# Performance work log

Hardware: AMD Instinct MI355X
Metric: run time of the kernel (lower is better)

Reference implementation:

```python
import jax, jax.numpy as jnp
import numpy as np

N_HEADS = 8
PROJ_DIM = 32


def _phi(x):
    # elu(x) + 1 feature map (always > 0)
    return jax.nn.elu(x) + 1.0


def _causal_linear(pq, pk, v):
    # Faithful to torch _linear_kernelized_attention masked branch:
    #   dpq_l = pq_l - pq_{l-1} (with pq_{-1}=0)
    #   result_l = cumsum_{m<=l} (dpq_m . v_m) * pk_m
    # The torch code materializes (N,H,L,D,D); here the identical math is
    # computed via a per-position scalar c_m = dpq_m . v_m, O(L*D) memory.
    dpq = pq - jnp.concatenate([jnp.zeros_like(pq[..., :1, :]), pq[..., :-1, :]], axis=-2)
    c = jnp.einsum('nhld,nhld->nhl', dpq, v)[..., None]  # (N,H,L,1)
    return jnp.cumsum(c * pk, axis=-2)  # (N,H,L,D)


def _bidir_linear(pq, pk, v):
    # Non-masked linear path: (pk^T v) first, then pq @ (.)
    right = jnp.einsum('nhld,nhle->nhde', pk, v)
    return jnp.einsum('nhqd,nhde->nhqe', pq, right)


def _attention(Y, X, Wq, Wk, Wv, mask):
    N, Lq, Dm = Y.shape
    Lk = X.shape[1]
    H, Pd = N_HEADS, PROJ_DIM
    # torch Linear: x @ W^T
    q = (Y @ Wq.T).reshape(N, Lq, H, Pd).transpose(0, 2, 1, 3)  # (N,H,Lq,Pd)
    k = (X @ Wk.T).reshape(N, Lk, H, Pd).transpose(0, 2, 1, 3)
    v = (X @ Wv.T).reshape(N, Lk, H, Pd).transpose(0, 2, 1, 3)
    pq, pk = _phi(q), _phi(k)
    fn = _causal_linear if mask else _bidir_linear
    num = fn(pq, pk, v)
    den = fn(pq, pk, jnp.ones_like(v))  # v_scale = ones expanded to D
    A = num / den
    return A.transpose(0, 2, 1, 3).reshape(N, Lq, H * Pd)


def setup_inputs() -> dict:
    key = jax.random.key(0)
    kY, kX, kq, kk, kv = jax.random.split(key, 5)
    N, L, dim = 2, 8192, N_HEADS * PROJ_DIM
    scale_in = 0.05            # keep phi(q),phi(k) ~ 1 so denominator stays positive
    scale_w = 1.0 / np.sqrt(dim)
    Y = scale_in * jax.random.normal(kY, (N, L, dim), dtype=jnp.float32)
    X = scale_in * jax.random.normal(kX, (N, L, dim), dtype=jnp.float32)
    Wq = scale_w * jax.random.normal(kq, (dim, dim), dtype=jnp.float32)
    Wk = scale_w * jax.random.normal(kk, (dim, dim), dtype=jnp.float32)
    Wv = scale_w * jax.random.normal(kv, (dim, dim), dtype=jnp.float32)
    return {"Y": Y, "X": X, "Wq": Wq, "Wk": Wk, "Wv": Wv, "mask": 1}


def reference(Y, X, Wq, Wk, Wv, mask):
    return _attention(Y, X, Wq, Wk, Wv, mask)
```

## Files before the change

### kernel.cpp

```cpp
#include <hip/hip_runtime.h>
#include <hip/hip_bf16.h>


typedef __attribute__((ext_vector_type(8))) short short8;
typedef __attribute__((ext_vector_type(4))) float f32x4;

__device__ __forceinline__ float phi_f(float x) {
    return x > 0.f ? x + 1.f : __expf(x);
}
__device__ __forceinline__ unsigned short f2bf(float x) {
    __hip_bfloat16 h = __float2bfloat16(x);
    return *reinterpret_cast<unsigned short*>(&h);
}
__device__ __forceinline__ float bf2f(unsigned short u) {
    return __uint_as_float(((unsigned int)u) << 16);
}

__global__ __launch_bounds__(256) void k_prepw(
        const float* __restrict__ Wq, const float* __restrict__ Wk,
        const float* __restrict__ Wv, unsigned short* __restrict__ Wf)
{
    const int g = blockIdx.x * 256 + threadIdx.x;
    const int mat = g >> 13, cc = g & 8191;
    const float* src = (mat == 0) ? Wq : (mat == 1 ? Wv : Wk);
    const int ln = cc & 15, qd = (cc >> 4) & 3, kt = (cc >> 6) & 7, jt = cc >> 9;
    const float* s = src + (size_t)(jt * 16 + ln) * 256 + kt * 32 + qd * 8;
    float4 f0 = *(const float4*)s, f1 = *(const float4*)(s + 4);
    short8 o;
    o[0] = f2bf(f0.x); o[1] = f2bf(f0.y); o[2] = f2bf(f0.z); o[3] = f2bf(f0.w);
    o[4] = f2bf(f1.x); o[5] = f2bf(f1.y); o[6] = f2bf(f1.z); o[7] = f2bf(f1.w);
    *(short8*)(Wf + (size_t)g * 8) = o;
}

#define LDA 280

__global__ __launch_bounds__(512, 4) void k_gemm(
        const float* __restrict__ Y, const float* __restrict__ X,
        const unsigned short* __restrict__ Wf,
        unsigned short* __restrict__ pk_out,
        float* __restrict__ c_out, float* __restrict__ cd_out,
        float* __restrict__ tot)
{
    __shared__ __align__(16) unsigned short Ys[33 * LDA];
    __shared__ __align__(16) unsigned short Xs[32 * LDA];
    __shared__ float scc[32][8], scd[32][8];
    __shared__ __align__(16) unsigned short spk[32 * 264];

    const int rb = blockIdx.x;
    const int n = rb >> 8, tile = rb & 255;
    const int mbase = rb * 32, lseg0 = tile * 32;
    const bool hasprev = (tile != 0);
    const int t = threadIdx.x, w = t >> 6, lane = t & 63;
    const int ln = lane & 15, qd = lane >> 4;

#pragma unroll
    for (int it = 0; it < 8; ++it) {
        const int idx = t + it * 512;
        const int half = idx >> 11, row = (idx >> 6) & 31, c4 = idx & 63;
        const float* s = (half ? X : Y) + (size_t)(mbase + row) * 256 + c4 * 4;
        float4 f = *(const float4*)s;
        ushort4 h4;
        h4.x = f2bf(f.x); h4.y = f2bf(f.y); h4.z = f2bf(f.z); h4.w = f2bf(f.w);
        unsigned short* dst = half ? Xs : Ys;
        *(ushort4*)&dst[row * LDA + c4 * 4] = h4;
    }
    if (t < 64) {
        const int prow = hasprev ? mbase - 1 : mbase;
        float4 f = *(const float4*)(Y + (size_t)prow * 256 + t * 4);
        ushort4 h4;
        h4.x = f2bf(f.x); h4.y = f2bf(f.y); h4.z = f2bf(f.z); h4.w = f2bf(f.w);
        *(ushort4*)&Ys[32 * LDA + t * 4] = h4;
    }
    __syncthreads();

    f32x4 aq[2][2], av[2][2], akk[2][2], aqp[2];
#pragma unroll
    for (int i = 0; i < 2; ++i)
#pragma unroll
        for (int j = 0; j < 2; ++j) {
            aq[i][j]  = (f32x4){0.f, 0.f, 0.f, 0.f};
            av[i][j]  = (f32x4){0.f, 0.f, 0.f, 0.f};
            akk[i][j] = (f32x4){0.f, 0.f, 0.f, 0.f};
        }
    aqp[0] = (f32x4){0.f, 0.f, 0.f, 0.f};
    aqp[1] = (f32x4){0.f, 0.f, 0.f, 0.f};
    const short8 z8 = {0, 0, 0, 0, 0, 0, 0, 0};
    const short8* W8 = (const short8*)Wf;

#pragma unroll
    for (int kt = 0; kt < 8; ++kt) {
        const int ko = kt * 32 + qd * 8;
        short8 ay0 = *(const short8*)&Ys[ln * LDA + ko];
        short8 ay1 = *(const short8*)&Ys[(16 + ln) * LDA + ko];
        short8 ax0 = *(const short8*)&Xs[ln * LDA + ko];
        short8 ax1 = *(const short8*)&Xs[(16 + ln) * LDA + ko];
        short8 ext = *(const short8*)&Ys[32 * LDA + ko];
        short8 ayp = (ln == 15) ? ext : z8;
#pragma unroll
        for (int jj = 0; jj < 2; ++jj) {
            const int jt = w * 2 + jj;
            short8 bq = W8[(((0 * 16 + jt) * 8 + kt) << 6) + lane];
            short8 bv = W8[(((1 * 16 + jt) * 8 + kt) << 6) + lane];
            short8 bk = W8[(((2 * 16 + jt) * 8 + kt) << 6) + lane];
            aq[0][jj]  = __builtin_amdgcn_mfma_f32_16x16x32_bf16(ay0, bq, aq[0][jj], 0, 0, 0);
            aq[1][jj]  = __builtin_amdgcn_mfma_f32_16x16x32_bf16(ay1, bq, aq[1][jj], 0, 0, 0);
            aqp[jj]    = __builtin_amdgcn_mfma_f32_16x16x32_bf16(ayp, bq, aqp[jj], 0, 0, 0);
            av[0][jj]  = __builtin_amdgcn_mfma_f32_16x16x32_bf16(ax0, bv, av[0][jj], 0, 0, 0);
            av[1][jj]  = __builtin_amdgcn_mfma_f32_16x16x32_bf16(ax1, bv, av[1][jj], 0, 0, 0);
            akk[0][jj] = __builtin_amdgcn_mfma_f32_16x16x32_bf16(ax0, bk, akk[0][jj], 0, 0, 0);
            akk[1][jj] = __builtin_amdgcn_mfma_f32_16x16x32_bf16(ax1, bk, akk[1][jj], 0, 0, 0);
        }
    }

#pragma unroll
    for (int i = 0; i < 2; ++i)
#pragma unroll
        for (int jj = 0; jj < 2; ++jj)
#pragma unroll
            for (int r = 0; r < 4; ++r) aq[i][jj][r] = phi_f(aq[i][jj][r]);
    float pprev[2];
#pragma unroll
    for (int jj = 0; jj < 2; ++jj) {
        float p15 = __shfl(aqp[jj][3], 48 + ln);
        pprev[jj] = hasprev ? phi_f(p15) : 0.f;
    }

    float cc_[2][4], cd_[2][4];
#pragma unroll
    for (int i = 0; i < 2; ++i)
#pragma unroll
        for (int r = 0; r < 4; ++r) { cc_[i][r] = 0.f; cd_[i][r] = 0.f; }
#pragma unroll
    for (int jj = 0; jj < 2; ++jj) {
        float carry = pprev[jj];
#pragma unroll
        for (int i = 0; i < 2; ++i) {
            const float p0 = aq[i][jj][0], p1 = aq[i][jj][1], p2 = aq[i][jj][2], p3 = aq[i][jj][3];
            const float up3 = __shfl_up(p3, 16);
            const float prev0 = (qd == 0) ? carry : up3;
            const float d0 = p0 - prev0, d1 = p1 - p0, d2 = p2 - p1, d3 = p3 - p2;
            cc_[i][0] += d0 * av[i][jj][0]; cd_[i][0] += d0;
            cc_[i][1] += d1 * av[i][jj][1]; cd_[i][1] += d1;
            cc_[i][2] += d2 * av[i][jj][2]; cd_[i][2] += d2;
            cc_[i][3] += d3 * av[i][jj][3]; cd_[i][3] += d3;
            carry = __shfl(p3, ln + 48);
        }
    }
#pragma unroll
    for (int i = 0; i < 2; ++i)
#pragma unroll
        for (int r = 0; r < 4; ++r) {
            float x = cc_[i][r];
            x += __shfl_xor(x, 1); x += __shfl_xor(x, 2);
            x += __shfl_xor(x, 4); x += __shfl_xor(x, 8);
            float y = cd_[i][r];
            y += __shfl_xor(y, 1); y += __shfl_xor(y, 2);
            y += __shfl_xor(y, 4); y += __shfl_xor(y, 8);
            if (ln == 0) {
                scc[i * 16 + qd * 4 + r][w] = x;
                scd[i * 16 + qd * 4 + r][w] = y;
            }
        }
    __syncthreads();
    {
        const int idx = t & 255, row = idx & 31, h = idx >> 5;
        const size_t gi = (size_t)(n * 8 + h) * 8192 + lseg0 + row;
        if (t < 256) c_out[gi]  = scc[row][h];
        else         cd_out[gi] = scd[row][h];
    }

#pragma unroll
    for (int i = 0; i < 2; ++i)
#pragma unroll
        for (int jj = 0; jj < 2; ++jj)
#pragma unroll
            for (int r = 0; r < 4; ++r) akk[i][jj][r] = phi_f(akk[i][jj][r]);
#pragma unroll
    for (int jj = 0; jj < 2; ++jj) {
        float tn = 0.f, td = 0.f;
#pragma unroll
        for (int i = 0; i < 2; ++i)
#pragma unroll
            for (int r = 0; r < 4; ++r) {
                const int row = i * 16 + qd * 4 + r;
                const float pv = akk[i][jj][r];
                tn += scc[row][w] * pv;
                td += scd[row][w] * pv;
            }
        tn += __shfl_xor(tn, 16); tn += __shfl_xor(tn, 32);
        td += __shfl_xor(td, 16); td += __shfl_xor(td, 32);
        if (qd == 0) {
            const int d = jj * 16 + ln;
            const size_t bi = ((size_t)(n * 8 + w) * 256 + tile) * 64;
            tot[bi + d]      = tn;
            tot[bi + 32 + d] = td;
        }
    }

#pragma unroll
    for (int i = 0; i < 2; ++i)
#pragma unroll
        for (int jj = 0; jj < 2; ++jj)
#pragma unroll
            for (int r = 0; r < 4; ++r)
                spk[(i * 16 + qd * 4 + r) * 264 + w * 32 + jj * 16 + ln] = f2bf(akk[i][jj][r]);
    __syncthreads();
#pragma unroll
    for (int it = 0; it < 2; ++it) {
        const int idx = t + 512 * it;
        const int row = idx >> 5, cg = idx & 31;
        short8 vals = *(const short8*)&spk[row * 264 + cg * 8];
        const int head = cg >> 2, d8 = (cg & 3) * 8;
        *(short8*)(pk_out + ((size_t)(n * 8 + head) * 8192 + lseg0 + row) * 32 + d8) = vals;
    }
}

__global__ __launch_bounds__(256) void k_scan(
        const unsigned short* __restrict__ pk, const float* __restrict__ c,
        const float* __restrict__ cd, const float* __restrict__ tot,
        float* __restrict__ out)
{
    __shared__ __align__(16) unsigned short spk[128 * 32];
    __shared__ float sc[128], sd[128];
    __shared__ float wsum[4][64], stile[4][64];

    const int bx = blockIdx.x, seg = bx >> 6, blk = bx & 63;
    const int n = seg >> 3, h = seg & 7;
    const int t = threadIdx.x, l0 = blk * 128;
    const int wv = t >> 6, lane = t & 63;
    const int T = blk * 4;

    const float* tb = tot + (size_t)seg * 256 * 64 + lane;
    float p0 = 0.f, p1 = 0.f, p2 = 0.f, p3 = 0.f,
          p4 = 0.f, p5 = 0.f, p6 = 0.f, p7 = 0.f;
    int i = wv;
    for (; i + 28 < T; i += 32) {
        p0 += tb[(i)      * 64]; p1 += tb[(i + 4)  * 64];
        p2 += tb[(i + 8)  * 64]; p3 += tb[(i + 12) * 64];
        p4 += tb[(i + 16) * 64]; p5 += tb[(i + 20) * 64];
        p6 += tb[(i + 24) * 64]; p7 += tb[(i + 28) * 64];
    }
    for (; i < T; i += 4) p0 += tb[i * 64];
    wsum[wv][lane]  = ((p0 + p1) + (p2 + p3)) + ((p4 + p5) + (p6 + p7));
    stile[wv][lane] = tb[(T + wv) * 64];

#pragma unroll
    for (int it = 0; it < 2; ++it) {
        const int idx = t + 256 * it;
        *(short8*)&spk[idx * 8] = *(const short8*)(pk + ((size_t)seg * 8192 + l0) * 32 + idx * 8);
    }
    if (t < 128) sc[t] = c[(size_t)seg * 8192 + l0 + t];
    else         sd[t - 128] = cd[(size_t)seg * 8192 + l0 + (t - 128)];
    __syncthreads();

    if (t < 128) {
        const int g = t >> 5, d = t & 31;
        float rn  = (wsum[0][d] + wsum[1][d]) + (wsum[2][d] + wsum[3][d]);
        float rd_ = (wsum[0][32 + d] + wsum[1][32 + d]) + (wsum[2][32 + d] + wsum[3][32 + d]);
#pragma unroll
        for (int i2 = 0; i2 < 3; ++i2)
            if (i2 < g) { rn += stile[i2][d]; rd_ += stile[i2][32 + d]; }
        float* ob = out + ((size_t)n * 8192 + l0 + g * 32) * 256 + h * 32 + d;
#pragma unroll
        for (int p = 0; p < 32; ++p) {
            const int m = g * 32 + p;
            const float pkv = bf2f(spk[m * 32 + d]);
            rn  += sc[m] * pkv;
            rd_ += sd[m] * pkv;
            ob[(size_t)p * 256] = rn / rd_;
        }
    }
}

extern "C" void kernel_launch(void* const* d_in, const int* in_sizes, int n_in,
                              void* d_out, int out_size, void* d_ws, size_t ws_size,
                              hipStream_t stream)
{
    const float* Y  = (const float*)d_in[0];
    const float* X  = (const float*)d_in[1];
    const float* Wq = (const float*)d_in[2];
    const float* Wk = (const float*)d_in[3];
    const float* Wv = (const float*)d_in[4];
    float* out = (float*)d_out;

    float* ws = (float*)d_ws;
    unsigned short* Wf = (unsigned short*)ws;
    unsigned short* pk = (unsigned short*)(ws + 98304);
    float* c   = ws + 98304 + 2097152;
    float* cd  = c  + 131072;
    float* tot = cd + 131072;

    hipLaunchKernelGGL(k_prepw, dim3(96),   dim3(256), 0, stream, Wq, Wk, Wv, Wf);
    hipLaunchKernelGGL(k_gemm,  dim3(512),  dim3(512), 0, stream,
                       Y, X, Wf, pk, c, cd, tot);
    hipLaunchKernelGGL(k_scan,  dim3(1024), dim3(256), 0, stream, pk, c, cd, tot, out);
}
```

Baseline: 112.0 us.

## Fuse projection GEMM and causal scan with cross-block flag-based prefix propagation

Merges the GEMM kernel and the scan kernel into one. Each block publishes its per-tile totals and sets a release flag, then waits on the flags of all earlier tiles in its sequence. It sums their totals to get its prefix and writes the final output directly from shared memory. This removes the pk/c/cd round trip through global memory and one kernel launch. In exchange it relies on all 512 blocks being co-resident to avoid deadlock, and later tiles serially re-read O(tile) totals.

```diff
diff --git a/kernel.cpp b/kernel.cpp
--- a/kernel.cpp
+++ b/kernel.cpp
@@ -34,17 +34,17 @@
 
 #define LDA 280
 
-__global__ __launch_bounds__(512, 4) void k_gemm(
+__global__ __launch_bounds__(512, 4) void k_fused(
         const float* __restrict__ Y, const float* __restrict__ X,
         const unsigned short* __restrict__ Wf,
-        unsigned short* __restrict__ pk_out,
-        float* __restrict__ c_out, float* __restrict__ cd_out,
-        float* __restrict__ tot)
+        float* __restrict__ tot_pub, int* __restrict__ flags,
+        float* __restrict__ out)
 {
     __shared__ __align__(16) unsigned short Ys[33 * LDA];
     __shared__ __align__(16) unsigned short Xs[32 * LDA];
     __shared__ float scc[32][8], scd[32][8];
     __shared__ __align__(16) unsigned short spk[32 * 264];
+    __shared__ float sprefix[512];
 
     const int rb = blockIdx.x;
     const int n = rb >> 8, tile = rb & 255;
@@ -162,12 +162,6 @@
             }
         }
     __syncthreads();
-    {
-        const int idx = t & 255, row = idx & 31, h = idx >> 5;
-        const size_t gi = (size_t)(n * 8 + h) * 8192 + lseg0 + row;
-        if (t < 256) c_out[gi]  = scc[row][h];
-        else         cd_out[gi] = scd[row][h];
-    }
 
 #pragma unroll
     for (int i = 0; i < 2; ++i)
@@ -191,9 +185,9 @@
         td += __shfl_xor(td, 16); td += __shfl_xor(td, 32);
         if (qd == 0) {
             const int d = jj * 16 + ln;
-            const size_t bi = ((size_t)(n * 8 + w) * 256 + tile) * 64;
-            tot[bi + d]      = tn;
-            tot[bi + 32 + d] = td;
+            const size_t bi = (size_t)rb * 512 + (size_t)w * 64;
+            tot_pub[bi + d]      = tn;
+            tot_pub[bi + 32 + d] = td;
         }
     }
 
@@ -205,69 +199,44 @@
             for (int r = 0; r < 4; ++r)
                 spk[(i * 16 + qd * 4 + r) * 264 + w * 32 + jj * 16 + ln] = f2bf(akk[i][jj][r]);
     __syncthreads();
-#pragma unroll
-    for (int it = 0; it < 2; ++it) {
-        const int idx = t + 512 * it;
-        const int row = idx >> 5, cg = idx & 31;
-        short8 vals = *(const short8*)&spk[row * 264 + cg * 8];
-        const int head = cg >> 2, d8 = (cg & 3) * 8;
-        *(short8*)(pk_out + ((size_t)(n * 8 + head) * 8192 + lseg0 + row) * 32 + d8) = vals;
-    }
-}
-
-__global__ __launch_bounds__(256) void k_scan(
-        const unsigned short* __restrict__ pk, const float* __restrict__ c,
-        const float* __restrict__ cd, const float* __restrict__ tot,
-        float* __restrict__ out)
-{
-    __shared__ __align__(16) unsigned short spk[128 * 32];
-    __shared__ float sc[128], sd[128];
-    __shared__ float wsum[4][64], stile[4][64];
-
-    const int bx = blockIdx.x, seg = bx >> 6, blk = bx & 63;
-    const int n = seg >> 3, h = seg & 7;
-    const int t = threadIdx.x, l0 = blk * 128;
-    const int wv = t >> 6, lane = t & 63;
-    const int T = blk * 4;
-
-    const float* tb = tot + (size_t)seg * 256 * 64 + lane;
-    float p0 = 0.f, p1 = 0.f, p2 = 0.f, p3 = 0.f,
-          p4 = 0.f, p5 = 0.f, p6 = 0.f, p7 = 0.f;
-    int i = wv;
-    for (; i + 28 < T; i += 32) {
-        p0 += tb[(i)      * 64]; p1 += tb[(i + 4)  * 64];
-        p2 += tb[(i + 8)  * 64]; p3 += tb[(i + 12) * 64];
-        p4 += tb[(i + 16) * 64]; p5 += tb[(i + 20) * 64];
-        p6 += tb[(i + 24) * 64]; p7 += tb[(i + 28) * 64];
-    }
-    for (; i < T; i += 4) p0 += tb[i * 64];
-    wsum[wv][lane]  = ((p0 + p1) + (p2 + p3)) + ((p4 + p5) + (p6 + p7));
-    stile[wv][lane] = tb[(T + wv) * 64];
-
-#pragma unroll
-    for (int it = 0; it < 2; ++it) {
-        const int idx = t + 256 * it;
-        *(short8*)&spk[idx * 8] = *(const short8*)(pk + ((size_t)seg * 8192 + l0) * 32 + idx * 8);
-    }
-    if (t < 128) sc[t] = c[(size_t)seg * 8192 + l0 + t];
-    else         sd[t - 128] = cd[(size_t)seg * 8192 + l0 + (t - 128)];
-    __syncthreads();
-
-    if (t < 128) {
-        const int g = t >> 5, d = t & 31;
-        float rn  = (wsum[0][d] + wsum[1][d]) + (wsum[2][d] + wsum[3][d]);
-        float rd_ = (wsum[0][32 + d] + wsum[1][32 + d]) + (wsum[2][32 + d] + wsum[3][32 + d]);
-#pragma unroll
-        for (int i2 = 0; i2 < 3; ++i2)
-            if (i2 < g) { rn += stile[i2][d]; rd_ += stile[i2][32 + d]; }
-        float* ob = out + ((size_t)n * 8192 + l0 + g * 32) * 256 + h * 32 + d;
-#pragma unroll
-        for (int p = 0; p < 32; ++p) {
-            const int m = g * 32 + p;
-            const float pkv = bf2f(spk[m * 32 + d]);
-            rn  += sc[m] * pkv;
-            rd_ += sd[m] * pkv;
-            ob[(size_t)p * 256] = rn / rd_;
+
+    if (t == 0) {
+        __threadfence();
+        __hip_atomic_store(&flags[rb], 1, __ATOMIC_RELEASE, __HIP_MEMORY_SCOPE_AGENT);
+    }
+
+    if (t < tile) {
+        while (__hip_atomic_load(&flags[rb - tile + t], __ATOMIC_ACQUIRE,
+                                 __HIP_MEMORY_SCOPE_AGENT) == 0)
+            __builtin_amdgcn_s_sleep(1);
+    }
+    __syncthreads();
+    __threadfence();
+
+    {
+        const float* tp = tot_pub + (size_t)(rb - tile) * 512 + t;
+        float a0 = 0.f, a1 = 0.f, a2 = 0.f, a3 = 0.f;
+        int i = 0;
+        for (; i + 3 < tile; i += 4) {
+            a0 += tp[(size_t)(i + 0) * 512]; a1 += tp[(size_t)(i + 1) * 512];
+            a2 += tp[(size_t)(i + 2) * 512]; a3 += tp[(size_t)(i + 3) * 512];
+        }
+        for (; i < tile; ++i) a0 += tp[(size_t)i * 512];
+        sprefix[t] = (a0 + a1) + (a2 + a3);
+    }
+    __syncthreads();
+
+    if (lane < 32) {
+        const int d = lane;
+        float rn  = sprefix[w * 64 + d];
+        float rd_ = sprefix[w * 64 + 32 + d];
+        float* ob = out + (size_t)(n * 8192 + lseg0) * 256 + w * 32 + d;
+#pragma unroll
+        for (int row = 0; row < 32; ++row) {
+            const float pkv = bf2f(spk[row * 264 + w * 32 + d]);
+            rn  += scc[row][w] * pkv;
+            rd_ += scd[row][w] * pkv;
+            ob[(size_t)row * 256] = rn / rd_;
         }
     }
 }
@@ -285,13 +254,11 @@
 
     float* ws = (float*)d_ws;
     unsigned short* Wf = (unsigned short*)ws;
-    unsigned short* pk = (unsigned short*)(ws + 98304);
-    float* c   = ws + 98304 + 2097152;
-    float* cd  = c  + 131072;
-    float* tot = cd + 131072;
-
-    hipLaunchKernelGGL(k_prepw, dim3(96),   dim3(256), 0, stream, Wq, Wk, Wv, Wf);
-    hipLaunchKernelGGL(k_gemm,  dim3(512),  dim3(512), 0, stream,
-                       Y, X, Wf, pk, c, cd, tot);
-    hipLaunchKernelGGL(k_scan,  dim3(1024), dim3(256), 0, stream, pk, c, cd, tot, out);
-}
+    float* tot_pub = ws + 98304;
+    int*   flags   = (int*)(ws + 98304 + 262144);
+
+    hipMemsetAsync(flags, 0, 512 * sizeof(int), stream);
+    hipLaunchKernelGGL(k_prepw, dim3(96),  dim3(256), 0, stream, Wq, Wk, Wv, Wf);
+    hipLaunchKernelGGL(k_fused, dim3(512), dim3(512), 0, stream,
+                       Y, X, Wf, tot_pub, flags, out);
+}
```

Result: slower. 219.8 us (+96.2%).
